# Kernel tuning notes

Measured on AMD Instinct MI355X. Metric: run time of the kernel, lower is better.

## Reference

```python
import jax, jax.numpy as jnp
import numpy as np

THRESHOLD = 0.005
EPS = 1e-5  # torch instance_norm default eps


def setup_inputs() -> dict:
    key = jax.random.key(0)
    k1, k2, k3 = jax.random.split(key, 3)
    B, C, H, W = 4, 64, 64, 64
    feat = 64
    stdv = 1.0 / np.sqrt(feat)  # matches __init_W_bias__ uniform(-stdv, stdv)
    x = jax.random.normal(k1, (B, C, H, W), dtype=jnp.float32)
    W0 = jax.random.uniform(k2, (1, feat, feat), dtype=jnp.float32, minval=-stdv, maxval=stdv)
    W1 = jax.random.uniform(k3, (1, feat, feat), dtype=jnp.float32, minval=-stdv, maxval=stdv)
    return {"x": x, "W0": W0, "W1": W1}


def _laplacian(xn):
    # xn: [B, N, C] node features (pixels x channels). Built under no_grad in torch.
    norms = jnp.sqrt(jnp.sum(xn * xn, axis=2, keepdims=True))  # [B, N, 1]
    num = jnp.einsum('bnc,bmc->bnm', xn, xn)                    # [B, N, N]
    corr = num / (norms * jnp.swapaxes(norms, 1, 2))
    # relu then threshold -> binary adjacency (threshold > 0, so relu is subsumed)
    A = (corr > THRESHOLD).astype(xn.dtype)
    deg = jnp.sum(A, axis=2)                                    # [B, N]
    d_is = 1.0 / jnp.sqrt(deg)                                  # inverse(sqrt(D)) is diagonal
    return A * d_is[:, :, None] * d_is[:, None, :]              # D^-1/2 A D^-1/2


def _instance_norm(h):
    # torch F.instance_norm on [B, N, F] normalizes over the last dim per (b, n)
    mean = jnp.mean(h, axis=-1, keepdims=True)
    var = jnp.mean((h - mean) ** 2, axis=-1, keepdims=True)
    return (h - mean) / jnp.sqrt(var + EPS)


def reference(x, W0, W1):
    B, C, H, Wd = x.shape
    x_linear = x.reshape(B, C, H * Wd).transpose(0, 2, 1)  # [B, N, C]
    lap = _laplacian(jax.lax.stop_gradient(x_linear))       # adjacency built with no_grad
    for Wk in (W0, W1):
        lx = jnp.einsum('bnm,bmc->bnc', lap, x_linear)      # laplacian diffusion
        h = jnp.einsum('bnc,cf->bnf', lx, Wk[0])            # shared weight (repeat over batch)
        x_linear = jax.nn.relu(_instance_norm(h))
    return x_linear
```

## Files before the change

### kernel.cpp

```cpp
#include <hip/hip_runtime.h>
#include <hip/hip_bf16.h>
#include <cstdint>

#define BB 4
#define CC 64
#define NN 4096
#define NWRD 64
#define TAU 0.005f
#define EPSN 1e-5f
#define MSPLITS 8

typedef __attribute__((ext_vector_type(8))) short short8;
typedef __attribute__((ext_vector_type(4))) float f32x4;
typedef unsigned long long ull;

__device__ inline unsigned int bf16_rne(float v) {
    unsigned int u = __float_as_uint(v);
    return (u + 0x7FFFu + ((u >> 16) & 1u)) >> 16;
}

__device__ inline void gload_lds16(const void* g, void* lds_base) {
    __builtin_amdgcn_global_load_lds(
        (const __attribute__((address_space(1))) unsigned int*)g,
        (__attribute__((address_space(3))) unsigned int*)lds_base, 16, 0, 0);
}

__global__ __launch_bounds__(256) void k_transpose(const float* __restrict__ x,
                                                   float* __restrict__ xt,
                                                   unsigned short* __restrict__ ynh,
                                                   unsigned short* __restrict__ ynl,
                                                   int* __restrict__ deg) {
    __shared__ float lds[64 * 65];
    int t = threadIdx.x;
    int b = blockIdx.y;
    int n0 = blockIdx.x * 64;
    int gid = (b * (NN / 64) + blockIdx.x) * 256 + t;
    if (gid < BB * NN) deg[gid] = 0;
    #pragma unroll
    for (int i = 0; i < 4; ++i) {
        int c = i * 16 + (t >> 4);
        int nc = (t & 15) * 4;
        float4 v = *(const float4*)(x + ((size_t)(b * CC + c)) * NN + n0 + nc);
        lds[c * 65 + nc + 0] = v.x;
        lds[c * 65 + nc + 1] = v.y;
        lds[c * 65 + nc + 2] = v.z;
        lds[c * 65 + nc + 3] = v.w;
    }
    __syncthreads();
    int l = t & 63, wv = t >> 6;
    for (int i = 0; i < 16; ++i) {
        int n = wv * 16 + i;
        float v = lds[l * 65 + n];
        float s = v * v;
        #pragma unroll
        for (int off = 32; off; off >>= 1) s += __shfl_xor(s, off, 64);
        float yv = v * rsqrtf(s);
        unsigned int hb = bf16_rne(yv);
        float lo = yv - __uint_as_float(hb << 16);
        unsigned int lb = bf16_rne(lo);
        size_t row = (size_t)(b * NN + n0 + n);
        xt[row * CC + l] = v;
        ynh[row * CC + l] = (unsigned short)hb;
        ynl[row * CC + l] = (unsigned short)lb;
    }
}

#define CORR_MC 128
__global__ __launch_bounds__(256) void k_corr(const unsigned short* __restrict__ ynh,
                                              const unsigned short* __restrict__ ynl,
                                              ull* __restrict__ mask,
                                              int* __restrict__ deg) {
    __shared__ unsigned short ldsH[2][CORR_MC * 64];
    __shared__ unsigned short ldsL[2][CORR_MC * 64];
    int t = threadIdx.x;
    int l = t & 63, wv = t >> 6;
    int lc = l & 15, q = l >> 4;
    int b = blockIdx.z;
    int idx = blockIdx.x, I = 0;
    while (idx >= 16 - I) { idx -= 16 - I; ++I; }
    int J = I + idx;
    int n0 = I * 256 + wv * 64;
    int m0 = J * 256;
    const unsigned short* bH = ynh + (size_t)b * NN * CC;
    const unsigned short* bL = ynl + (size_t)b * NN * CC;

    short8 ah[4][2], al[4][2];
    #pragma unroll
    for (int nt = 0; nt < 4; ++nt)
        #pragma unroll
        for (int ks = 0; ks < 2; ++ks) {
            size_t off = (size_t)(n0 + nt * 16 + lc) * CC + (ks * 4 + q) * 8;
            ah[nt][ks] = *(const short8*)(bH + off);
            al[nt][ks] = *(const short8*)(bL + off);
        }

    int rr = l & 15;
    int rsel = rr & 3;
    int qq = rr >> 2;
    int myq = l >> 4;

    auto stage = [&](int mc, int bufi) {
        int mbase = m0 + mc * CORR_MC;
        #pragma unroll
        for (int rd = 0; rd < 4; ++rd) {
            int gu = rd * 256 + wv * 64;
            int g = gu + l;
            int ci = (g & ~7) | ((g & 7) ^ ((g >> 3) & 7));
            gload_lds16(bH + (size_t)mbase * CC + ci * 8, &ldsH[bufi][gu * 8]);
            gload_lds16(bL + (size_t)mbase * CC + ci * 8, &ldsL[bufi][gu * 8]);
        }
    };

    ull wout[4];
    int degacc = 0;
    stage(0, 0);
    for (int mc = 0; mc < 2; ++mc) {
        __syncthreads();
        if (mc == 0) stage(1, 1);
        int bufi = mc & 1;
        ull w0 = 0, w1 = 0;
        #pragma unroll
        for (int tt = 0; tt < 8; ++tt) {
            short8 bh[2], bl[2];
            #pragma unroll
            for (int ks = 0; ks < 2; ++ks) {
                int rowm = tt * 16 + lc;
                int sw = ((ks * 4 + q) ^ (rowm & 7)) * 8;
                bh[ks] = *(const short8*)&ldsH[bufi][rowm * 64 + sw];
                bl[ks] = *(const short8*)&ldsL[bufi][rowm * 64 + sw];
            }
            #pragma unroll
            for (int nt = 0; nt < 4; ++nt) {
                f32x4 acc = {0.f, 0.f, 0.f, 0.f};
                #pragma unroll
                for (int ks = 0; ks < 2; ++ks) {
                    acc = __builtin_amdgcn_mfma_f32_16x16x32_bf16(ah[nt][ks], bh[ks], acc, 0, 0, 0);
                    acc = __builtin_amdgcn_mfma_f32_16x16x32_bf16(ah[nt][ks], bl[ks], acc, 0, 0, 0);
                    acc = __builtin_amdgcn_mfma_f32_16x16x32_bf16(al[nt][ks], bh[ks], acc, 0, 0, 0);
                }
                ull bal[4];
                #pragma unroll
                for (int r = 0; r < 4; ++r)
                    bal[r] = __ballot(acc[r] > TAU);
                ull sa = (rsel & 1) ? bal[1] : bal[0];
                ull sb = (rsel & 1) ? bal[3] : bal[2];
                ull sel = (rsel & 2) ? sb : sa;
                ull part = ((sel >> (qq * 16)) & 0xFFFFull) << ((tt & 3) * 16);
                if (myq == nt) { if (tt < 4) w0 |= part; else w1 |= part; }
            }
        }
        wout[mc * 2 + 0] = w0;
        wout[mc * 2 + 1] = w1;
        degacc += __popcll(w0) + __popcll(w1);
    }

    int row = b * NN + n0 + l;
    ull* mdst = mask + (size_t)row * NWRD + J * 4;
    #pragma unroll
    for (int c = 0; c < 4; ++c) mdst[c] = wout[c];
    atomicAdd(&deg[row], degacc);

    if (J > I) {
        __syncthreads();
        ull* sh = (ull*)&ldsH[0][0];
        #pragma unroll
        for (int c = 0; c < 4; ++c) sh[(wv * 64 + l) * 5 + c] = wout[c];
        __syncthreads();
        const ull Mv[6] = {0x00000000FFFFFFFFull, 0x0000FFFF0000FFFFull,
                           0x00FF00FF00FF00FFull, 0x0F0F0F0F0F0F0F0Full,
                           0x3333333333333333ull, 0x5555555555555555ull};
        int dm = 0;
        ull tw[4];
        #pragma unroll
        for (int a = 0; a < 4; ++a) {
            ull xv = sh[(a * 64 + l) * 5 + wv];
            int dd = 32;
            #pragma unroll
            for (int s = 0; s < 6; ++s, dd >>= 1) {
                ull y = __shfl_xor(xv, dd, 64);
                ull M = Mv[s];
                xv = (l & dd) ? ((xv & ~M) | ((y >> dd) & M))
                              : ((xv & M) | ((y << dd) & ~M));
            }
            tw[a] = xv;
            dm += __popcll(xv);
        }
        int mrow = b * NN + J * 256 + wv * 64 + l;
        #pragma unroll
        for (int a = 0; a < 4; ++a)
            mask[(size_t)mrow * NWRD + I * 4 + a] = tw[a];
        atomicAdd(&deg[mrow], dm);
    }
}

__global__ __launch_bounds__(256) void k_pack(const float* __restrict__ xin,
                                              const int* __restrict__ deg,
                                              unsigned short* __restrict__ yph) {
    __shared__ float lds[32 * 65];
    int t = threadIdx.x;
    int kt = blockIdx.x;
    int b = blockIdx.y;
    size_t ibase = (size_t)b * NN * CC + (size_t)kt * 32 * CC;
    #pragma unroll
    for (int i = 0; i < 2; ++i) {
        int f4 = i * 256 + t;
        int m = f4 >> 4;
        float d = rsqrtf((float)deg[b * NN + kt * 32 + m]);
        float4 v = ((const float4*)(xin + ibase))[f4];
        int c = (f4 & 15) * 4;
        lds[m * 65 + c + 0] = v.x * d;
        lds[m * 65 + c + 1] = v.y * d;
        lds[m * 65 + c + 2] = v.z * d;
        lds[m * 65 + c + 3] = v.w * d;
    }
    __syncthreads();
    size_t obase = (size_t)b * NN * CC + (size_t)kt * 2048;
    int kin = t & 31;
    int chi = t >> 5;
    #pragma unroll
    for (int cg = 0; cg < 8; ++cg) {
        int c = cg * 8 + chi;
        yph[obase + c * 32 + kin] = (unsigned short)bf16_rne(lds[kin * 65 + c]);
    }
}

#define GMC 128
__global__ __launch_bounds__(256) void k_gemm(const ull* __restrict__ mask,
                                              const unsigned short* __restrict__ yph,
                                              float* __restrict__ plx) {
    __shared__ unsigned short ldsB[2][4 * 2048];
    int t = threadIdx.x;
    int l = t & 63, wv = t >> 6;
    int lc = l & 15, q = l >> 4;
    int b = blockIdx.z;
    int ms = blockIdx.y;
    int n0 = blockIdx.x * 256 + wv * 64;
    int m0 = ms * 512;
    const unsigned short* src = yph + (size_t)b * NN * CC;

    ull mw[4][4][2];
    #pragma unroll
    for (int nt = 0; nt < 4; ++nt) {
        const ull* mrow = mask + ((size_t)(b * NN + n0 + nt * 16 + lc)) * NWRD + (m0 >> 6);
        #pragma unroll
        for (int mc = 0; mc < 4; ++mc) {
            mw[mc][nt][0] = mrow[mc * 2];
            mw[mc][nt][1] = mrow[mc * 2 + 1];
        }
    }

    f32x4 acc[4][4];
    #pragma unroll
    for (int nt = 0; nt < 4; ++nt)
        #pragma unroll
        for (int tt = 0; tt < 4; ++tt) acc[nt][tt] = f32x4{0.f, 0.f, 0.f, 0.f};

    auto stage = [&](int mc, int bufi) {
        int ktbase = (m0 + mc * GMC) >> 5;
        #pragma unroll
        for (int rd = 0; rd < 4; ++rd) {
            int gu = rd * 256 + wv * 64;
            gload_lds16(src + (size_t)ktbase * 2048 + (gu + l) * 8, &ldsB[bufi][gu * 8]);
        }
    };

    stage(0, 0);
    for (int mc = 0; mc < 4; ++mc) {
        __syncthreads();
        if (mc + 1 < 4) stage(mc + 1, (mc + 1) & 1);
        int bufi = mc & 1;
        #pragma unroll
        for (int kt = 0; kt < 4; ++kt) {
            int sh = (kt & 1) * 32 + q * 8;
            union { unsigned int u[4]; short8 v; } a[4];
            #pragma unroll
            for (int nt = 0; nt < 4; ++nt) {
                unsigned int bits = (unsigned int)(mw[mc][nt][kt >> 1] >> sh) & 0xFFu;
                #pragma unroll
                for (int j = 0; j < 4; ++j)
                    a[nt].u[j] = ((bits >> (2 * j)) & 1u ? 0x3F80u : 0u)
                               | ((bits >> (2 * j + 1)) & 1u ? 0x3F800000u : 0u);
            }
            #pragma unroll
            for (int tt = 0; tt < 4; ++tt) {
                short8 bf = *(const short8*)&ldsB[bufi][kt * 2048 + (tt * 16 + lc) * 32 + q * 8];
                #pragma unroll
                for (int nt = 0; nt < 4; ++nt)
                    acc[nt][tt] = __builtin_amdgcn_mfma_f32_16x16x32_bf16(a[nt].v, bf, acc[nt][tt], 0, 0, 0);
            }
        }
    }
    #pragma unroll
    for (int nt = 0; nt < 4; ++nt)
        #pragma unroll
        for (int tt = 0; tt < 4; ++tt)
            #pragma unroll
            for (int r = 0; r < 4; ++r) {
                int n = n0 + nt * 16 + q * 4 + r;
                int c = tt * 16 + lc;
                plx[((size_t)((ms * BB + b)) * NN + n) * CC + c] = acc[nt][tt][r];
            }
}

__global__ __launch_bounds__(256) void k_out(const float* __restrict__ plx,
                                             const int* __restrict__ deg,
                                             const float* __restrict__ W,
                                             float* __restrict__ xout,
                                             unsigned short* __restrict__ xpack) {
    __shared__ float lxs[4][68];
    int lane = threadIdx.x & 63;
    int wave = threadIdx.x >> 6;
    int b = blockIdx.y;
    int n0 = blockIdx.x * 16 + wave * 4;
    float Wreg[64];
    #pragma unroll
    for (int c = 0; c < 64; ++c) Wreg[c] = W[c * 64 + lane];
    for (int tI = 0; tI < 4; ++tI) {
        int n = n0 + tI;
        size_t row = (size_t)(b * NN + n);
        float dRow = rsqrtf((float)deg[row]);
        float lx = 0.f;
        #pragma unroll
        for (int s = 0; s < MSPLITS; ++s)
            lx += plx[((size_t)(s * BB + b) * NN + n) * CC + lane];
        lx *= dRow;
        lxs[wave][lane] = lx;
        float h = 0.f;
        #pragma unroll
        for (int c4 = 0; c4 < 16; ++c4) {
            float4 s4 = *(const float4*)&lxs[wave][c4 * 4];
            h += s4.x * Wreg[c4 * 4 + 0] + s4.y * Wreg[c4 * 4 + 1]
               + s4.z * Wreg[c4 * 4 + 2] + s4.w * Wreg[c4 * 4 + 3];
        }
        float mean = h;
        #pragma unroll
        for (int off = 32; off; off >>= 1) mean += __shfl_xor(mean, off, 64);
        mean *= (1.f / 64.f);
        float dv = h - mean;
        float var = dv * dv;
        #pragma unroll
        for (int off = 32; off; off >>= 1) var += __shfl_xor(var, off, 64);
        var *= (1.f / 64.f);
        float o = dv * rsqrtf(var + EPSN);
        o = o > 0.f ? o : 0.f;
        if (xout)
            xout[row * CC + lane] = o;
        if (xpack)
            xpack[(size_t)b * NN * CC + (size_t)(n >> 5) * 2048 + lane * 32 + (n & 31)] =
                (unsigned short)bf16_rne(o * dRow);
    }
}

extern "C" void kernel_launch(void* const* d_in, const int* in_sizes, int n_in,
                              void* d_out, int out_size, void* d_ws, size_t ws_size,
                              hipStream_t stream) {
    const float* x  = (const float*)d_in[0];
    const float* W0 = (const float*)d_in[1];
    const float* W1 = (const float*)d_in[2];
    float* out = (float*)d_out;

    char* ws = (char*)d_ws;
    ull* mask = (ull*)(ws);
    float* xt = (float*)(ws + ((size_t)8 << 20));
    unsigned short* ynh = (unsigned short*)(ws + ((size_t)12 << 20));
    unsigned short* ynl = (unsigned short*)(ws + ((size_t)14 << 20));
    unsigned short* xp0 = (unsigned short*)(ws + ((size_t)16 << 20));
    unsigned short* xp1 = (unsigned short*)(ws + ((size_t)18 << 20));
    float* plx = (float*)(ws + ((size_t)20 << 20));
    int* deg = (int*)(ws + ((size_t)52 << 20));

    k_transpose<<<dim3(NN / 64, BB), 256, 0, stream>>>(x, xt, ynh, ynl, deg);
    k_corr<<<dim3(136, 1, BB), 256, 0, stream>>>(ynh, ynl, mask, deg);

    k_pack<<<dim3(128, BB), 256, 0, stream>>>(xt, deg, xp0);
    k_gemm<<<dim3(NN / 256, MSPLITS, BB), 256, 0, stream>>>(mask, xp0, plx);
    k_out<<<dim3(NN / 16, BB), 256, 0, stream>>>(plx, deg, W0, nullptr, xp1);

    k_gemm<<<dim3(NN / 256, MSPLITS, BB), 256, 0, stream>>>(mask, xp1, plx);
    k_out<<<dim3(NN / 16, BB), 256, 0, stream>>>(plx, deg, W1, out, nullptr);
}
```

Before: 152.9 us.

## Fuse masked Laplacian GEMM with output projection and instance norm

Measured after the change: 144.3 us. 1.06x faster.

```diff
diff --git a/kernel.cpp b/kernel.cpp
--- a/kernel.cpp
+++ b/kernel.cpp
@@ -8,7 +8,6 @@
 #define NWRD 64
 #define TAU 0.005f
 #define EPSN 1e-5f
-#define MSPLITS 8
 
 typedef __attribute__((ext_vector_type(8))) short short8;
 typedef __attribute__((ext_vector_type(4))) float f32x4;
@@ -224,29 +223,38 @@
     }
 }
 
-#define GMC 128
-__global__ __launch_bounds__(256) void k_gemm(const ull* __restrict__ mask,
-                                              const unsigned short* __restrict__ yph,
-                                              float* __restrict__ plx) {
-    __shared__ unsigned short ldsB[2][4 * 2048];
+__global__ __launch_bounds__(512, 2) void k_fused(const ull* __restrict__ mask,
+                                                  const unsigned short* __restrict__ yph,
+                                                  const int* __restrict__ deg,
+                                                  const float* __restrict__ W,
+                                                  float* __restrict__ xout,
+                                                  unsigned short* __restrict__ xpack) {
+    __shared__ __align__(16) unsigned char smem[8 * 64 * 68 * 4];
+    unsigned short* ldsB = (unsigned short*)smem;
+    float (*red)[68] = (float (*)[68])smem;
+
     int t = threadIdx.x;
     int l = t & 63, wv = t >> 6;
     int lc = l & 15, q = l >> 4;
-    int b = blockIdx.z;
-    int ms = blockIdx.y;
-    int n0 = blockIdx.x * 256 + wv * 64;
-    int m0 = ms * 512;
+    int b = blockIdx.y;
+    int n0 = blockIdx.x * 64;
     const unsigned short* src = yph + (size_t)b * NN * CC;
 
-    ull mw[4][4][2];
+    auto stage = [&](int ch, int bufi) {
+        int g0 = wv * 16 + ch * 2;
+        #pragma unroll
+        for (int r = 0; r < 8; ++r)
+            gload_lds16(src + (size_t)g0 * 2048 + r * 512 + l * 8,
+                        &ldsB[bufi * 32768 + wv * 4096 + r * 512]);
+    };
+    stage(0, 0);
+
+    ull mw[8][4];
     #pragma unroll
     for (int nt = 0; nt < 4; ++nt) {
-        const ull* mrow = mask + ((size_t)(b * NN + n0 + nt * 16 + lc)) * NWRD + (m0 >> 6);
-        #pragma unroll
-        for (int mc = 0; mc < 4; ++mc) {
-            mw[mc][nt][0] = mrow[mc * 2];
-            mw[mc][nt][1] = mrow[mc * 2 + 1];
-        }
+        const ull* mrow = mask + ((size_t)(b * NN + n0 + nt * 16 + lc)) * NWRD + wv * 8;
+        #pragma unroll
+        for (int ch = 0; ch < 8; ++ch) mw[ch][nt] = mrow[ch];
     }
 
     f32x4 acc[4][4];
@@ -255,27 +263,17 @@
         #pragma unroll
         for (int tt = 0; tt < 4; ++tt) acc[nt][tt] = f32x4{0.f, 0.f, 0.f, 0.f};
 
-    auto stage = [&](int mc, int bufi) {
-        int ktbase = (m0 + mc * GMC) >> 5;
-        #pragma unroll
-        for (int rd = 0; rd < 4; ++rd) {
-            int gu = rd * 256 + wv * 64;
-            gload_lds16(src + (size_t)ktbase * 2048 + (gu + l) * 8, &ldsB[bufi][gu * 8]);
-        }
-    };
-
-    stage(0, 0);
-    for (int mc = 0; mc < 4; ++mc) {
+    #pragma unroll
+    for (int ch = 0; ch < 8; ++ch) {
         __syncthreads();
-        if (mc + 1 < 4) stage(mc + 1, (mc + 1) & 1);
-        int bufi = mc & 1;
-        #pragma unroll
-        for (int kt = 0; kt < 4; ++kt) {
-            int sh = (kt & 1) * 32 + q * 8;
+        if (ch + 1 < 8) stage(ch + 1, (ch + 1) & 1);
+        const unsigned short* bbase = &ldsB[(ch & 1) * 32768 + wv * 4096];
+        #pragma unroll
+        for (int kt = 0; kt < 2; ++kt) {
             union { unsigned int u[4]; short8 v; } a[4];
             #pragma unroll
             for (int nt = 0; nt < 4; ++nt) {
-                unsigned int bits = (unsigned int)(mw[mc][nt][kt >> 1] >> sh) & 0xFFu;
+                unsigned int bits = (unsigned int)(mw[ch][nt] >> (kt * 32 + q * 8)) & 0xFFu;
                 #pragma unroll
                 for (int j = 0; j < 4; ++j)
                     a[nt].u[j] = ((bits >> (2 * j)) & 1u ? 0x3F80u : 0u)
@@ -283,52 +281,51 @@
             }
             #pragma unroll
             for (int tt = 0; tt < 4; ++tt) {
-                short8 bf = *(const short8*)&ldsB[bufi][kt * 2048 + (tt * 16 + lc) * 32 + q * 8];
+                short8 bf = *(const short8*)&bbase[kt * 2048 + (tt * 16 + lc) * 32 + q * 8];
                 #pragma unroll
                 for (int nt = 0; nt < 4; ++nt)
                     acc[nt][tt] = __builtin_amdgcn_mfma_f32_16x16x32_bf16(a[nt].v, bf, acc[nt][tt], 0, 0, 0);
             }
         }
     }
+
+    __syncthreads();
     #pragma unroll
     for (int nt = 0; nt < 4; ++nt)
         #pragma unroll
         for (int tt = 0; tt < 4; ++tt)
             #pragma unroll
-            for (int r = 0; r < 4; ++r) {
-                int n = n0 + nt * 16 + q * 4 + r;
-                int c = tt * 16 + lc;
-                plx[((size_t)((ms * BB + b)) * NN + n) * CC + c] = acc[nt][tt][r];
-            }
-}
-
-__global__ __launch_bounds__(256) void k_out(const float* __restrict__ plx,
-                                             const int* __restrict__ deg,
-                                             const float* __restrict__ W,
-                                             float* __restrict__ xout,
-                                             unsigned short* __restrict__ xpack) {
-    __shared__ float lxs[4][68];
-    int lane = threadIdx.x & 63;
-    int wave = threadIdx.x >> 6;
-    int b = blockIdx.y;
-    int n0 = blockIdx.x * 16 + wave * 4;
+            for (int r = 0; r < 4; ++r)
+                red[wv * 64 + nt * 16 + q * 4 + r][tt * 16 + lc] = acc[nt][tt][r];
+    __syncthreads();
+
+    {
+        int n = t >> 3, c0 = (t & 7) * 8;
+        float dRow = rsqrtf((float)deg[b * NN + n0 + n]);
+        float s[8] = {0.f, 0.f, 0.f, 0.f, 0.f, 0.f, 0.f, 0.f};
+        #pragma unroll
+        for (int w = 0; w < 8; ++w) {
+            const float* rp = &red[w * 64 + n][c0];
+            #pragma unroll
+            for (int j = 0; j < 8; ++j) s[j] += rp[j];
+        }
+        float* wp = &red[n][c0];
+        #pragma unroll
+        for (int j = 0; j < 8; ++j) wp[j] = s[j] * dRow;
+    }
+    __syncthreads();
+
     float Wreg[64];
     #pragma unroll
-    for (int c = 0; c < 64; ++c) Wreg[c] = W[c * 64 + lane];
-    for (int tI = 0; tI < 4; ++tI) {
-        int n = n0 + tI;
-        size_t row = (size_t)(b * NN + n);
-        float dRow = rsqrtf((float)deg[row]);
-        float lx = 0.f;
-        #pragma unroll
-        for (int s = 0; s < MSPLITS; ++s)
-            lx += plx[((size_t)(s * BB + b) * NN + n) * CC + lane];
-        lx *= dRow;
-        lxs[wave][lane] = lx;
+    for (int c = 0; c < 64; ++c) Wreg[c] = W[c * 64 + l];
+    #pragma unroll
+    for (int tI = 0; tI < 8; ++tI) {
+        int nn = wv * 8 + tI;
+        int grow = b * NN + n0 + nn;
         float h = 0.f;
         #pragma unroll
         for (int c4 = 0; c4 < 16; ++c4) {
-            float4 s4 = *(const float4*)&lxs[wave][c4 * 4];
+            float4 s4 = *(const float4*)&red[nn][c4 * 4];
             h += s4.x * Wreg[c4 * 4 + 0] + s4.y * Wreg[c4 * 4 + 1]
                + s4.z * Wreg[c4 * 4 + 2] + s4.w * Wreg[c4 * 4 + 3];
         }
@@ -344,10 +341,13 @@
         float o = dv * rsqrtf(var + EPSN);
         o = o > 0.f ? o : 0.f;
         if (xout)
-            xout[row * CC + lane] = o;
-        if (xpack)
-            xpack[(size_t)b * NN * CC + (size_t)(n >> 5) * 2048 + lane * 32 + (n & 31)] =
-                (unsigned short)bf16_rne(o * dRow);
+            xout[(size_t)grow * CC + l] = o;
+        if (xpack) {
+            float dR = rsqrtf((float)deg[grow]);
+            int ng = n0 + nn;
+            xpack[(size_t)b * NN * CC + (size_t)(ng >> 5) * 2048 + l * 32 + (ng & 31)] =
+                (unsigned short)bf16_rne(o * dR);
+        }
     }
 }
 
@@ -366,16 +366,13 @@
     unsigned short* ynl = (unsigned short*)(ws + ((size_t)14 << 20));
     unsigned short* xp0 = (unsigned short*)(ws + ((size_t)16 << 20));
     unsigned short* xp1 = (unsigned short*)(ws + ((size_t)18 << 20));
-    float* plx = (float*)(ws + ((size_t)20 << 20));
-    int* deg = (int*)(ws + ((size_t)52 << 20));
+    int* deg = (int*)(ws + ((size_t)20 << 20));
 
     k_transpose<<<dim3(NN / 64, BB), 256, 0, stream>>>(x, xt, ynh, ynl, deg);
     k_corr<<<dim3(136, 1, BB), 256, 0, stream>>>(ynh, ynl, mask, deg);
 
     k_pack<<<dim3(128, BB), 256, 0, stream>>>(xt, deg, xp0);
-    k_gemm<<<dim3(NN / 256, MSPLITS, BB), 256, 0, stream>>>(mask, xp0, plx);
-    k_out<<<dim3(NN / 16, BB), 256, 0, stream>>>(plx, deg, W0, nullptr, xp1);
-
-    k_gemm<<<dim3(NN / 256, MSPLITS, BB), 256, 0, stream>>>(mask, xp1, plx);
-    k_out<<<dim3(NN / 16, BB), 256, 0, stream>>>(plx, deg, W1, out, nullptr);
-}
+    k_fused<<<dim3(NN / 64, BB), 512, 0, stream>>>(mask, xp0, deg, W0, nullptr, xp1);
+
+    k_fused<<<dim3(NN / 64, BB), 512, 0, stream>>>(mask, xp1, deg, W1, out, nullptr);
+}
```
